# Performance work log

Measured on AMD Instinct MI355X. Metric: run time of the kernel, lower is better.

## Reference

```python
import jax, jax.numpy as jnp
import numpy as np

ALPHA = 0.2  # LeakyReLU negative slope
NEG_INF = -1e9


def setup_inputs() -> dict:
    key = jax.random.key(0)
    k1, k2, k3, k4 = jax.random.split(key, 4)
    B, N, F_in, F_out = 4, 4096, 128, 128
    h = jax.random.normal(k1, (B, N, F_in), dtype=jnp.float32)
    adj = jax.random.randint(k2, (B, N, N), 0, 2, dtype=jnp.int32)
    # Xavier-uniform init matching nn.Linear weights
    limW = np.sqrt(6.0 / (F_in + F_out))
    W = jax.random.uniform(k3, (F_in, F_out), jnp.float32, -limW, limW)
    lima = np.sqrt(6.0 / (2 * F_out + 1))
    a = jax.random.uniform(k4, (2 * F_out,), jnp.float32, -lima, lima)
    return {"h": h, "adj": adj, "W": W, "a": a}


def reference(h, adj, W, a):
    # h: (B, N, F_in), adj: (B, N, N) int, W: (F_in, F_out), a: (2*F_out,)
    F_out = W.shape[1]
    Wh = jnp.einsum("bnf,fo->bno", h, W)  # (B, N, F_out)
    a_i, a_j = a[:F_out], a[F_out:]
    # e_ij = leakyrelu(a . [Wh_i, Wh_j]) = leakyrelu(a_i.Wh_i + a_j.Wh_j)
    si = Wh @ a_i  # (B, N) contribution of destination node i
    sj = Wh @ a_j  # (B, N) contribution of source node j
    e = si[:, :, None] + sj[:, None, :]  # (B, N, N)
    e = jnp.where(e > 0, e, ALPHA * e)  # LeakyReLU
    e = jnp.where(adj > 0, e, NEG_INF)  # masked scores
    attention = jax.nn.softmax(e, axis=-1)  # (B, N, N)
    # dropout is identity in eval mode
    h_prime = jnp.einsum("bij,bjo->bio", attention, Wh)  # (B, N, F_out)
    return jax.nn.elu(h_prime)  # concat=True -> ELU
```

## Files before the change

kernel.cpp:

```cpp
#include <hip/hip_runtime.h>

#define GN 4096
#define GF 128
#define GB 4

typedef __attribute__((ext_vector_type(8))) short short8;
typedef __attribute__((ext_vector_type(4))) float floatx4;

static __device__ __forceinline__ unsigned short f2bf(float x){
  unsigned int u = __float_as_uint(x);
  u += 0x7FFFu + ((u >> 16) & 1u);
  return (unsigned short)(u >> 16);
}

__global__ __launch_bounds__(256)
void gat_prep(const float* __restrict__ h, const float* __restrict__ W,
              const float* __restrict__ a, unsigned short* __restrict__ whB,
              float* __restrict__ si_g, unsigned short* __restrict__ EFh)
{
  __shared__ float hl[16*GF];
  __shared__ float red[2][2][16];
  const int tid = threadIdx.x;
  const int b   = blockIdx.x >> 8;
  const int r0  = (blockIdx.x & 255) << 4;
  const int o = tid & 127, g = tid >> 7;

  const float4* hb4 = (const float4*)(h + ((size_t)(b*GN + r0))*GF);
  ((float4*)hl)[tid]       = hb4[tid];
  ((float4*)hl)[tid + 256] = hb4[tid + 256];
  __syncthreads();

  float acc[8];
  #pragma unroll
  for (int r=0;r<8;++r) acc[r] = 0.f;
  const float* Wp = W + o;
  for (int f4=0; f4<32; ++f4){
    const float w0 = Wp[(f4*4+0)*GF];
    const float w1 = Wp[(f4*4+1)*GF];
    const float w2 = Wp[(f4*4+2)*GF];
    const float w3 = Wp[(f4*4+3)*GF];
    #pragma unroll
    for (int r=0;r<8;++r){
      const float4 h4 = *(const float4*)&hl[((g<<3)+r)*GF + (f4<<2)];
      acc[r] = fmaf(h4.x, w0, acc[r]);
      acc[r] = fmaf(h4.y, w1, acc[r]);
      acc[r] = fmaf(h4.z, w2, acc[r]);
      acc[r] = fmaf(h4.w, w3, acc[r]);
    }
  }

  const float ai = a[o], aj = a[GF + o];
  const int lane = tid & 63, wh = (tid >> 6) & 1;
  #pragma unroll
  for (int r=0;r<8;++r){
    float vi = acc[r]*ai, vj = acc[r]*aj;
    #pragma unroll
    for (int off=32; off; off>>=1){ vi += __shfl_down(vi, off); vj += __shfl_down(vj, off); }
    if (lane == 0){ red[0][wh][(g<<3)+r] = vi; red[1][wh][(g<<3)+r] = vj; }
  }

  unsigned short us[8] __attribute__((aligned(16)));
  #pragma unroll
  for (int r=0;r<8;++r) us[r] = f2bf(acc[r]);
  {
    const int j0 = r0 + (g<<3);
    unsigned short* dst = whB + (((size_t)(b*128 + (j0>>5))*128 + o)<<5) + (j0&31);
    *(uint4*)dst = *(const uint4*)us;
  }

  __syncthreads();
  if (tid < 16){
    si_g[b*GN + r0 + tid] = red[0][0][tid] + red[0][1][tid];
  } else if (tid < 32){
    const int r = tid - 16;
    const float vsj = red[1][0][r] + red[1][1][r];
    EFh[(size_t)b*8192 + r0 + r]        = f2bf(__expf(vsj));
    EFh[(size_t)b*8192 + 4096 + r0 + r] = f2bf(__expf(0.2f*vsj));
  }
}

__global__ __launch_bounds__(256, 2)
void gat_main(const int* __restrict__ adj, const unsigned short* __restrict__ whB,
              const float* __restrict__ si_g, const unsigned short* __restrict__ EFh,
              float* __restrict__ out)
{
  __shared__ __align__(16) char smem[16384 + 32*134*4];
  unsigned short* sEj = (unsigned short*)smem;
  unsigned int*   bitsW  = (unsigned int*)(smem + 16384);
  unsigned long long* bits64 = (unsigned long long*)(smem + 16384);
  float* smemc = (float*)smem;

  const int tid  = threadIdx.x;
  const int wave = tid >> 6, lane = tid & 63;
  const int b  = (blockIdx.x >> 1) & 3;
  const int i0 = ((((blockIdx.x >> 3) << 1) | (blockIdx.x & 1))) << 5;
  const int m = lane & 15, quad = lane >> 4, q8 = quad << 3;

  const int jw = wave << 10, jw32 = wave << 5;

  {
    const uint4* Eg = (const uint4*)(EFh + (size_t)b*8192);
    uint4* sE4 = (uint4*)sEj;
    #pragma unroll
    for (int k=0;k<4;++k) sE4[tid + (k<<8)] = Eg[tid + (k<<8)];
  }

  {
    const int* adjb = adj + ((size_t)(b*GN + i0))*GN + jw;
    #pragma unroll 2
    for (int r = 0; r < 32; ++r){
      const int* src = adjb + (size_t)r*GN;
      int v[16];
      #pragma unroll
      for (int c = 0; c < 16; ++c)
        v[c] = __builtin_nontemporal_load(src + (c<<6) + lane);
      #pragma unroll
      for (int c = 0; c < 16; ++c){
        const unsigned long long mm = __ballot(v[c] > 0);
        if (lane == 0) bits64[r*67 + (wave<<4) + c] = mm;
      }
    }
  }
  __syncthreads();

  const float si0 = si_g[(size_t)b*GN + i0 + m];
  const float si1 = si_g[(size_t)b*GN + i0 + 16 + m];
  const float Ti0 = __expf(-si0),      Ti1 = __expf(-si1);
  const float Ri0 = __expf(-0.8f*si0), Ri1 = __expf(-0.8f*si1);
  const unsigned short* lanebase = whB + ((size_t)b<<19) + (m<<5) + q8;

  floatx4 acc0[8], acc1[8];
  #pragma unroll
  for (int c=0;c<8;++c){ acc0[c] = (floatx4){0.f,0.f,0.f,0.f}; acc1[c] = (floatx4){0.f,0.f,0.f,0.f}; }
  floatx4 lf0 = (floatx4){0.f,0.f,0.f,0.f}, lf1 = (floatx4){0.f,0.f,0.f,0.f};
  const short8 ones8 = {0x3F80,0x3F80,0x3F80,0x3F80,0x3F80,0x3F80,0x3F80,0x3F80};

#define MKAF(dst_, sh_, Ti_, Ri_) do { \
    unsigned int aw[4]; \
    _Pragma("unroll") \
    for (int p=0;p<4;++p){ \
      unsigned int e0 = Eu[p] << 16, e1 = Eu[p] & 0xFFFF0000u; \
      unsigned int f0 = Fu[p] << 16, f1 = Fu[p] & 0xFFFF0000u; \
      float E0 = __uint_as_float(e0), E1 = __uint_as_float(e1); \
      float t0 = (Ri_)*__uint_as_float(f0), t1 = (Ri_)*__uint_as_float(f1); \
      float p0 = (E0 > (Ti_)) ? E0 : t0; \
      float p1 = (E1 > (Ti_)) ? E1 : t1; \
      unsigned int k0 = (unsigned int)(((int)((sh_) << (31-(2*p))))   >> 31); \
      unsigned int k1 = (unsigned int)(((int)((sh_) << (31-(2*p+1)))) >> 31); \
      unsigned int b0 = __float_as_uint(p0) & k0; \
      unsigned int b1 = __float_as_uint(p1) & k1; \
      aw[p] = ((b0 + 0x8000u) >> 16) | ((b1 + 0x8000u) & 0xFFFF0000u); \
    } \
    dst_ = *(const short8*)aw; \
  } while(0)

  #pragma unroll 2
  for (int it = 0; it < 32; ++it){
    const unsigned short* wb = lanebase + ((size_t)(jw32+it)<<12);
    short8 Bc[8];
    #pragma unroll
    for (int c=0;c<8;++c) Bc[c] = *(const short8*)(wb + (c<<9));

    const unsigned int sh0 = bitsW[m*134 + jw32 + it] >> q8;
    const unsigned int sh1 = bitsW[(m+16)*134 + jw32 + it] >> q8;
    const int jj = jw + (it << 5) + q8;
    const short8 Es = *(const short8*)&sEj[jj];
    const short8 Fs = *(const short8*)&sEj[4096 + jj];
    const unsigned int* Eu = (const unsigned int*)&Es;
    const unsigned int* Fu = (const unsigned int*)&Fs;
    short8 af0, af1;
    MKAF(af0, sh0, Ti0, Ri0);
    MKAF(af1, sh1, Ti1, Ri1);
    #pragma unroll
    for (int c=0;c<8;++c){
      acc0[c] = __builtin_amdgcn_mfma_f32_16x16x32_bf16(af0, Bc[c], acc0[c], 0, 0, 0);
      acc1[c] = __builtin_amdgcn_mfma_f32_16x16x32_bf16(af1, Bc[c], acc1[c], 0, 0, 0);
    }
    lf0 = __builtin_amdgcn_mfma_f32_16x16x32_bf16(af0, ones8, lf0, 0, 0, 0);
    lf1 = __builtin_amdgcn_mfma_f32_16x16x32_bf16(af1, ones8, lf1, 0, 0, 0);
  }
#undef MKAF

  #pragma unroll 1
  for (int g = 0; g < 2; ++g){
    __syncthreads();
    #pragma unroll
    for (int c=0;c<8;++c){
      #pragma unroll
      for (int r=0;r<4;++r){
        const float v = g ? acc1[c][r] : acc0[c][r];
        smemc[(wave*16 + quad*4 + r)*129 + c*16 + m] = v;
      }
    }
    if (m == 0){
      #pragma unroll
      for (int r=0;r<4;++r) smemc[8256 + wave*16 + quad*4 + r] = g ? lf1[r] : lf0[r];
    }
    __syncthreads();

    #pragma unroll
    for (int k=0;k<8;++k){
      const int idx = tid + (k<<8);
      const int row = idx >> 7, col = idx & 127;
      const float s = smemc[row*129+col] + smemc[(16+row)*129+col]
                    + smemc[(32+row)*129+col] + smemc[(48+row)*129+col];
      const float l = smemc[8256+row] + smemc[8256+16+row]
                    + smemc[8256+32+row] + smemc[8256+48+row];
      float v = s / l;
      v = v > 0.f ? v : expm1f(v);
      out[((size_t)(b*GN + i0 + (g<<4) + row))*GF + col] = v;
    }
  }
}

extern "C" void kernel_launch(void* const* d_in, const int* in_sizes, int n_in,
                              void* d_out, int out_size, void* d_ws, size_t ws_size,
                              hipStream_t stream)
{
  (void)in_sizes; (void)n_in; (void)out_size; (void)ws_size;
  const float* h   = (const float*)d_in[0];
  const int*   adj = (const int*)d_in[1];
  const float* W   = (const float*)d_in[2];
  const float* a   = (const float*)d_in[3];
  float* out = (float*)d_out;

  char* ws = (char*)d_ws;
  unsigned short* whB   = (unsigned short*)ws;
  float*          si    = (float*)(ws + (size_t)4*1024*1024);
  unsigned short* EFh   = (unsigned short*)(ws + (size_t)4*1024*1024 + 64*1024);

  gat_prep<<<GB*GN/16, 256, 0, stream>>>(h, W, a, whB, si, EFh);
  gat_main<<<GB*GN/32, 256, 0, stream>>>(adj, whB, si, EFh, out);
}
```

Measured before the change: 407.9 us.

## Double gat_main row tile to 64 rows with 512-thread blocks

Each gat_main block now handles 64 destination rows with 8 waves instead of 32 rows with 4 waves. Each wave covers half as many source columns but holds four 16-row accumulator groups, so every loaded Wh B-fragment feeds twice as many MFMAs. This halves the total global reads of the bf16 Wh operand across the grid. The cross-wave reduction gains an extra accumulate pass in shared memory. Holding 4x8 accumulators plus B fragments within the register budget of launch_bounds(512,2) risks register spills or lower occupancy.

```diff
diff --git a/kernel.cpp b/kernel.cpp
--- a/kernel.cpp
+++ b/kernel.cpp
@@ -79,12 +79,12 @@
   }
 }
 
-__global__ __launch_bounds__(256, 2)
+__global__ __launch_bounds__(512, 2)
 void gat_main(const int* __restrict__ adj, const unsigned short* __restrict__ whB,
               const float* __restrict__ si_g, const unsigned short* __restrict__ EFh,
               float* __restrict__ out)
 {
-  __shared__ __align__(16) char smem[16384 + 32*134*4];
+  __shared__ __align__(16) char smem[16384 + 64*67*8];
   unsigned short* sEj = (unsigned short*)smem;
   unsigned int*   bitsW  = (unsigned int*)(smem + 16384);
   unsigned long long* bits64 = (unsigned long long*)(smem + 16384);
@@ -93,46 +93,53 @@
   const int tid  = threadIdx.x;
   const int wave = tid >> 6, lane = tid & 63;
   const int b  = (blockIdx.x >> 1) & 3;
-  const int i0 = ((((blockIdx.x >> 3) << 1) | (blockIdx.x & 1))) << 5;
+  const int i0 = ((((blockIdx.x >> 3) << 1) | (blockIdx.x & 1))) << 6;
   const int m = lane & 15, quad = lane >> 4, q8 = quad << 3;
 
-  const int jw = wave << 10, jw32 = wave << 5;
+  const int jw = wave << 9, jw32 = wave << 4;
 
   {
     const uint4* Eg = (const uint4*)(EFh + (size_t)b*8192);
     uint4* sE4 = (uint4*)sEj;
-    #pragma unroll
-    for (int k=0;k<4;++k) sE4[tid + (k<<8)] = Eg[tid + (k<<8)];
+    sE4[tid]       = Eg[tid];
+    sE4[tid + 512] = Eg[tid + 512];
   }
 
   {
     const int* adjb = adj + ((size_t)(b*GN + i0))*GN + jw;
     #pragma unroll 2
-    for (int r = 0; r < 32; ++r){
+    for (int r = 0; r < 64; ++r){
       const int* src = adjb + (size_t)r*GN;
-      int v[16];
-      #pragma unroll
-      for (int c = 0; c < 16; ++c)
+      int v[8];
+      #pragma unroll
+      for (int c = 0; c < 8; ++c)
         v[c] = __builtin_nontemporal_load(src + (c<<6) + lane);
       #pragma unroll
-      for (int c = 0; c < 16; ++c){
+      for (int c = 0; c < 8; ++c){
         const unsigned long long mm = __ballot(v[c] > 0);
-        if (lane == 0) bits64[r*67 + (wave<<4) + c] = mm;
+        if (lane == 0) bits64[r*67 + (wave<<3) + c] = mm;
       }
     }
   }
   __syncthreads();
 
-  const float si0 = si_g[(size_t)b*GN + i0 + m];
-  const float si1 = si_g[(size_t)b*GN + i0 + 16 + m];
-  const float Ti0 = __expf(-si0),      Ti1 = __expf(-si1);
-  const float Ri0 = __expf(-0.8f*si0), Ri1 = __expf(-0.8f*si1);
+  float Ti[4], Ri[4];
+  #pragma unroll
+  for (int g=0; g<4; ++g){
+    const float siv = si_g[(size_t)b*GN + i0 + (g<<4) + m];
+    Ti[g] = __expf(-siv);
+    Ri[g] = __expf(-0.8f*siv);
+  }
   const unsigned short* lanebase = whB + ((size_t)b<<19) + (m<<5) + q8;
 
-  floatx4 acc0[8], acc1[8];
-  #pragma unroll
-  for (int c=0;c<8;++c){ acc0[c] = (floatx4){0.f,0.f,0.f,0.f}; acc1[c] = (floatx4){0.f,0.f,0.f,0.f}; }
-  floatx4 lf0 = (floatx4){0.f,0.f,0.f,0.f}, lf1 = (floatx4){0.f,0.f,0.f,0.f};
+  floatx4 acc[4][8];
+  floatx4 lf[4];
+  #pragma unroll
+  for (int g=0;g<4;++g){
+    #pragma unroll
+    for (int c=0;c<8;++c) acc[g][c] = (floatx4){0.f,0.f,0.f,0.f};
+    lf[g] = (floatx4){0.f,0.f,0.f,0.f};
+  }
   const short8 ones8 = {0x3F80,0x3F80,0x3F80,0x3F80,0x3F80,0x3F80,0x3F80,0x3F80};
 
 #define MKAF(dst_, sh_, Ti_, Ri_) do { \
@@ -155,52 +162,71 @@
   } while(0)
 
   #pragma unroll 2
-  for (int it = 0; it < 32; ++it){
+  for (int it = 0; it < 16; ++it){
     const unsigned short* wb = lanebase + ((size_t)(jw32+it)<<12);
     short8 Bc[8];
     #pragma unroll
     for (int c=0;c<8;++c) Bc[c] = *(const short8*)(wb + (c<<9));
 
-    const unsigned int sh0 = bitsW[m*134 + jw32 + it] >> q8;
-    const unsigned int sh1 = bitsW[(m+16)*134 + jw32 + it] >> q8;
     const int jj = jw + (it << 5) + q8;
     const short8 Es = *(const short8*)&sEj[jj];
     const short8 Fs = *(const short8*)&sEj[4096 + jj];
     const unsigned int* Eu = (const unsigned int*)&Es;
     const unsigned int* Fu = (const unsigned int*)&Fs;
-    short8 af0, af1;
-    MKAF(af0, sh0, Ti0, Ri0);
-    MKAF(af1, sh1, Ti1, Ri1);
+
+    short8 af[4];
+    #pragma unroll
+    for (int g=0;g<4;++g){
+      const unsigned int sh = bitsW[(m + (g<<4))*134 + jw32 + it] >> q8;
+      MKAF(af[g], sh, Ti[g], Ri[g]);
+    }
     #pragma unroll
     for (int c=0;c<8;++c){
-      acc0[c] = __builtin_amdgcn_mfma_f32_16x16x32_bf16(af0, Bc[c], acc0[c], 0, 0, 0);
-      acc1[c] = __builtin_amdgcn_mfma_f32_16x16x32_bf16(af1, Bc[c], acc1[c], 0, 0, 0);
-    }
-    lf0 = __builtin_amdgcn_mfma_f32_16x16x32_bf16(af0, ones8, lf0, 0, 0, 0);
-    lf1 = __builtin_amdgcn_mfma_f32_16x16x32_bf16(af1, ones8, lf1, 0, 0, 0);
+      #pragma unroll
+      for (int g=0;g<4;++g)
+        acc[g][c] = __builtin_amdgcn_mfma_f32_16x16x32_bf16(af[g], Bc[c], acc[g][c], 0, 0, 0);
+    }
+    #pragma unroll
+    for (int g=0;g<4;++g)
+      lf[g] = __builtin_amdgcn_mfma_f32_16x16x32_bf16(af[g], ones8, lf[g], 0, 0, 0);
   }
 #undef MKAF
 
   #pragma unroll 1
-  for (int g = 0; g < 2; ++g){
+  for (int g = 0; g < 4; ++g){
     __syncthreads();
-    #pragma unroll
-    for (int c=0;c<8;++c){
-      #pragma unroll
-      for (int r=0;r<4;++r){
-        const float v = g ? acc1[c][r] : acc0[c][r];
-        smemc[(wave*16 + quad*4 + r)*129 + c*16 + m] = v;
-      }
-    }
-    if (m == 0){
-      #pragma unroll
-      for (int r=0;r<4;++r) smemc[8256 + wave*16 + quad*4 + r] = g ? lf1[r] : lf0[r];
+    if (wave >= 4){
+      #pragma unroll
+      for (int c=0;c<8;++c){
+        #pragma unroll
+        for (int r=0;r<4;++r)
+          smemc[((wave-4)*16 + quad*4 + r)*129 + c*16 + m] = acc[g][c][r];
+      }
+      if (m == 0){
+        #pragma unroll
+        for (int r=0;r<4;++r) smemc[8256 + (wave-4)*16 + quad*4 + r] = lf[g][r];
+      }
     }
     __syncthreads();
-
-    #pragma unroll
-    for (int k=0;k<8;++k){
-      const int idx = tid + (k<<8);
+    if (wave < 4){
+      #pragma unroll
+      for (int c=0;c<8;++c){
+        #pragma unroll
+        for (int r=0;r<4;++r){
+          const int idx = (wave*16 + quad*4 + r)*129 + c*16 + m;
+          smemc[idx] += acc[g][c][r];
+        }
+      }
+      if (m == 0){
+        #pragma unroll
+        for (int r=0;r<4;++r) smemc[8256 + wave*16 + quad*4 + r] += lf[g][r];
+      }
+    }
+    __syncthreads();
+
+    #pragma unroll
+    for (int k=0;k<4;++k){
+      const int idx = tid + (k<<9);
       const int row = idx >> 7, col = idx & 127;
       const float s = smemc[row*129+col] + smemc[(16+row)*129+col]
                     + smemc[(32+row)*129+col] + smemc[(48+row)*129+col];
@@ -230,5 +256,5 @@
   unsigned short* EFh   = (unsigned short*)(ws + (size_t)4*1024*1024 + 64*1024);
 
   gat_prep<<<GB*GN/16, 256, 0, stream>>>(h, W, a, whB, si, EFh);
-  gat_main<<<GB*GN/32, 256, 0, stream>>>(adj, whB, si, EFh, out);
-}
+  gat_main<<<GB*GN/64, 512, 0, stream>>>(adj, whB, si, EFh, out);
+}
```

New measurement: 426.5 us. 4.6% more time.
